# Optimization experiments

Hardware: AMD Instinct MI355X
Metric: run time of the kernel (lower is better)

The kernel has to match this reference:

```python
import jax, jax.numpy as jnp
import numpy as np

SEG_T = 0.7      # segmentation_map_threshold
GAUSS_T = 0.7    # gaussian_segmentation_threshold
EPS = 1e-07
PI_APPROX = 3.14  # literal used in the original code


def setup_inputs() -> dict:
    key = jax.random.key(0)
    k1, k2 = jax.random.split(key)
    B, H, W = 2, 80, 80
    variance_map = jax.random.normal(k1, (B, 3, H, W), dtype=jnp.float32)
    segmentation_map = jax.random.uniform(k2, (B, 1, H, W), dtype=jnp.float32)
    return {"variance_map": variance_map, "segmentation_map": segmentation_map}


def _splat_single(var, seg):
    # var: [3,H,W], seg: [H,W]
    H, W = seg.shape
    mask = (seg > SEG_T).reshape(-1)                      # [P], P = H*W (candidate points)
    vh = jnp.square(var[0].reshape(-1))                   # variance_height^2
    vw = jnp.square(var[1].reshape(-1))                   # variance_width^2
    th = PI_APPROX * jax.nn.sigmoid(var[2].reshape(-1))
    s, c = jnp.sin(th), jnp.cos(th)
    a = c * c / (2 * vh + EPS) + s * s / (2 * vw + EPS)
    b = -2 * s * c / (4 * vh + EPS) + 2 * s * c / (4 * vw + EPS)
    cc = s * s / (2 * vh + EPS) + c * c / (2 * vw + EPS)
    p = jnp.arange(H * W)
    x = (p // W).astype(jnp.float32)                      # row coordinate of each point
    y = (p % W).astype(jnp.float32)                       # col coordinate of each point
    ig, jg = jnp.meshgrid(jnp.arange(H, dtype=jnp.float32),
                          jnp.arange(W, dtype=jnp.float32), indexing="ij")
    di = ig[None, :, :] - x[:, None, None] + EPS          # [P,H,W]
    dj = jg[None, :, :] - y[:, None, None] + EPS          # [P,H,W]
    g = jnp.exp(-(a[:, None, None] * di * di
                  + b[:, None, None] * 2.0 * di * dj
                  + cc[:, None, None] * dj * dj) + EPS)   # [P,H,W]
    # zero out gaussians from points below the segmentation threshold;
    # since exp(.) > 0, this exactly matches max over only the nonzero points
    g = jnp.where(mask[:, None, None], g, 0.0)
    gmax = jnp.max(g, axis=0)                             # [H,W]
    return (gmax >= GAUSS_T).astype(gmax.dtype) * gmax


def reference(variance_map, segmentation_map):
    out = jax.vmap(_splat_single)(variance_map, segmentation_map[:, 0])  # [B,H,W]
    return out[:, None, :, :]                                            # [B,1,H,W]
```

## Files before the change

kernel.cpp:

```cpp
#include <hip/hip_runtime.h>
#include <math.h>

#define HGT 80
#define WID 80
#define HW 6400
#define SEG_T 0.7f
#define GAUSS_T 0.7f
#define EPSF 1e-7f
#define PI_APPROX 3.14f
#define EXP_CLAMP 85.0f
#define QKEEP 0.5f

#define NTHR 512
#define NWV  8
#define NIT  13

__global__ void __launch_bounds__(NTHR)
fused_kernel(const float* __restrict__ var, const float* __restrict__ seg,
             float* __restrict__ out) {
    __shared__ float qred[NWV][64];

    const int tid  = threadIdx.x;
    const int lane = tid & 63;
    const int wv   = tid >> 6;
    const int t    = blockIdx.x;
    const int b    = blockIdx.y;
    const int ti = t / 10, tj = t - ti * 10;
    const int pr = ti * 8 + (lane >> 3);
    const int pc = tj * 8 + (lane & 7);
    const float fi = (float)pr, fj = (float)pc;
    const float ii = fi * fi, ij = fi * fj, jj = fj * fj;
    const float tr0 = (float)(ti * 8), tr1 = (float)(ti * 8 + 7);
    const float tc0 = (float)(tj * 8), tc1 = (float)(tj * 8 + 7);

    const float* vb = var + (size_t)b * 3 * HW;
    const float* sg = seg + (size_t)b * HW;

    float qmin = 3.0e38f;

    for (int c = 0; c < NIT; ++c) {
        const int p = c * NTHR + tid;
        float C0, C1, C2, C3, C4, C5;
        bool keep = false;

        if (p < HW && sg[p] > SEG_T) {
            const float v0 = vb[p], v1 = vb[HW + p];
            const float vh = v0 * v0, vw = v1 * v1;
            const int rr = p / WID, ccol = p - rr * WID;
            const float x = (float)rr, y = (float)ccol;
            const float dx = fmaxf(0.0f, fmaxf(tr0 - x, x - tr1));
            const float dy = fmaxf(0.0f, fmaxf(tc0 - y, y - tc1));
            const float d2 = dx * dx + dy * dy;
            if (d2 <= QKEEP * (2.0f * fmaxf(vh, vw) + EPSF)) {
                const float v2 = vb[2 * HW + p];
                const float th = PI_APPROX * (1.0f / (1.0f + expf(-v2)));
                const float sn = sinf(th), cs = cosf(th);
                const float A  = cs * cs / (2.0f * vh + EPSF) + sn * sn / (2.0f * vw + EPSF);
                const float Bb = -2.0f * sn * cs / (4.0f * vh + EPSF)
                               +  2.0f * sn * cs / (4.0f * vw + EPSF);
                const float Cc = sn * sn / (2.0f * vh + EPSF) + cs * cs / (2.0f * vw + EPSF);
                const float B2 = 2.0f * Bb;
                const float u = EPSF - x;
                const float v = EPSF - y;
                C0 = A;
                C1 = B2;
                C2 = Cc;
                C3 = 2.0f * A * u + B2 * v;
                C4 = B2 * u + 2.0f * Cc * v;
                C5 = A * u * u + B2 * u * v + Cc * v * v;
                keep = true;
            }
        }

        unsigned long long msk = __ballot(keep);
        while (msk) {
            int s = (int)__builtin_ctzll(msk);
            msk &= msk - 1;
            float c0 = __shfl(C0, s), c1 = __shfl(C1, s);
            float c2 = __shfl(C2, s), c3 = __shfl(C3, s);
            float c4 = __shfl(C4, s), c5 = __shfl(C5, s);
            float Q = fmaf(c0, ii,
                      fmaf(c1, ij,
                      fmaf(c2, jj,
                      fmaf(c3, fi,
                      fmaf(c4, fj, c5)))));
            qmin = fminf(qmin, Q);
        }
    }

    qred[wv][lane] = qmin;
    __syncthreads();
    if (wv == 0) {
        float m2 = qred[0][lane];
        #pragma unroll
        for (int w = 1; w < NWV; ++w) m2 = fminf(m2, qred[w][lane]);
        float g = expf(fminf(EPSF - m2, EXP_CLAMP));
        out[(size_t)b * HW + pr * WID + pc] = (g >= GAUSS_T) ? g : 0.0f;
    }
}

extern "C" void kernel_launch(void* const* d_in, const int* in_sizes, int n_in,
                              void* d_out, int out_size, void* d_ws, size_t ws_size,
                              hipStream_t stream) {
    const float* var = (const float*)d_in[0];
    const float* seg = (const float*)d_in[1];
    float* out = (float*)d_out;
    int B = in_sizes[1] / HW;
    dim3 grid(100, B);
    fused_kernel<<<grid, NTHR, 0, stream>>>(var, seg, out);
}
```

Baseline: 63.84 us.

## Compact kept points into LDS list and compute coefficients densely per wave

Each wave first preloads seg and variance values for all its candidate points, then filters them and stream-compacts the survivors into a per-wave shared-memory index list using ballot and popcount. Gaussian coefficients are then computed once per batch of 64 kept points with full lane utilisation, replacing the sparse per-iteration divergent coefficient computation. The extra cost is shared memory (about 26KB for the list), more registers for the preloaded arrays, and a second gather of the variance values.

```diff
diff --git a/kernel.cpp b/kernel.cpp
--- a/kernel.cpp
+++ b/kernel.cpp
@@ -14,10 +14,12 @@
 #define NTHR 512
 #define NWV  8
 #define NIT  13
+#define QCAP (NIT*64)
 
 __global__ void __launch_bounds__(NTHR)
 fused_kernel(const float* __restrict__ var, const float* __restrict__ seg,
              float* __restrict__ out) {
+    __shared__ int   qlist[NWV][QCAP];
     __shared__ float qred[NWV][64];
 
     const int tid  = threadIdx.x;
@@ -36,54 +38,74 @@
     const float* vb = var + (size_t)b * 3 * HW;
     const float* sg = seg + (size_t)b * HW;
 
-    float qmin = 3.0e38f;
+    float sgv[NIT], av0[NIT], av1[NIT];
+    #pragma unroll
+    for (int c = 0; c < NIT; ++c) {
+        const int p  = c * NTHR + tid;
+        const int pk = (p < HW) ? p : (HW - 1);
+        sgv[c] = sg[pk];
+        av0[c] = vb[pk];
+        av1[c] = vb[HW + pk];
+    }
 
+    int qn = 0;
+    #pragma unroll
     for (int c = 0; c < NIT; ++c) {
         const int p = c * NTHR + tid;
-        float C0, C1, C2, C3, C4, C5;
         bool keep = false;
-
-        if (p < HW && sg[p] > SEG_T) {
-            const float v0 = vb[p], v1 = vb[HW + p];
-            const float vh = v0 * v0, vw = v1 * v1;
+        if (p < HW && sgv[c] > SEG_T) {
+            const float vh = av0[c] * av0[c], vw = av1[c] * av1[c];
             const int rr = p / WID, ccol = p - rr * WID;
             const float x = (float)rr, y = (float)ccol;
             const float dx = fmaxf(0.0f, fmaxf(tr0 - x, x - tr1));
             const float dy = fmaxf(0.0f, fmaxf(tc0 - y, y - tc1));
             const float d2 = dx * dx + dy * dy;
-            if (d2 <= QKEEP * (2.0f * fmaxf(vh, vw) + EPSF)) {
-                const float v2 = vb[2 * HW + p];
-                const float th = PI_APPROX * (1.0f / (1.0f + expf(-v2)));
-                const float sn = sinf(th), cs = cosf(th);
-                const float A  = cs * cs / (2.0f * vh + EPSF) + sn * sn / (2.0f * vw + EPSF);
-                const float Bb = -2.0f * sn * cs / (4.0f * vh + EPSF)
-                               +  2.0f * sn * cs / (4.0f * vw + EPSF);
-                const float Cc = sn * sn / (2.0f * vh + EPSF) + cs * cs / (2.0f * vw + EPSF);
-                const float B2 = 2.0f * Bb;
-                const float u = EPSF - x;
-                const float v = EPSF - y;
-                C0 = A;
-                C1 = B2;
-                C2 = Cc;
-                C3 = 2.0f * A * u + B2 * v;
-                C4 = B2 * u + 2.0f * Cc * v;
-                C5 = A * u * u + B2 * u * v + Cc * v * v;
-                keep = true;
+            keep = d2 <= QKEEP * (2.0f * fmaxf(vh, vw) + EPSF);
+        }
+        const unsigned long long msk = __ballot(keep);
+        if (msk) {
+            if (keep) {
+                const int idx = qn + (int)__popcll(msk & ((1ull << lane) - 1ull));
+                qlist[wv][idx] = p;
             }
+            qn += (int)__popcll(msk);
         }
+    }
 
-        unsigned long long msk = __ballot(keep);
-        while (msk) {
-            int s = (int)__builtin_ctzll(msk);
-            msk &= msk - 1;
-            float c0 = __shfl(C0, s), c1 = __shfl(C1, s);
-            float c2 = __shfl(C2, s), c3 = __shfl(C3, s);
-            float c4 = __shfl(C4, s), c5 = __shfl(C5, s);
-            float Q = fmaf(c0, ii,
-                      fmaf(c1, ij,
-                      fmaf(c2, jj,
-                      fmaf(c3, fi,
-                      fmaf(c4, fj, c5)))));
+    float qmin = 3.0e38f;
+    for (int base = 0; base < qn; base += 64) {
+        const int nb = min(64, qn - base);
+        float C0 = 0, C1 = 0, C2 = 0, C3 = 0, C4 = 0, C5 = 0;
+        if (lane < nb) {
+            const int p = qlist[wv][base + lane];
+            const float v0 = vb[p], v1 = vb[HW + p], v2 = vb[2 * HW + p];
+            const float vh = v0 * v0, vw = v1 * v1;
+            const float th = PI_APPROX * (1.0f / (1.0f + expf(-v2)));
+            const float sn = sinf(th), cs = cosf(th);
+            const float A  = cs * cs / (2.0f * vh + EPSF) + sn * sn / (2.0f * vw + EPSF);
+            const float Bb = -2.0f * sn * cs / (4.0f * vh + EPSF)
+                           +  2.0f * sn * cs / (4.0f * vw + EPSF);
+            const float Cc = sn * sn / (2.0f * vh + EPSF) + cs * cs / (2.0f * vw + EPSF);
+            const float B2 = 2.0f * Bb;
+            const int rr = p / WID, ccol = p - rr * WID;
+            const float u = EPSF - (float)rr;
+            const float v = EPSF - (float)ccol;
+            C0 = A;
+            C1 = B2;
+            C2 = Cc;
+            C3 = 2.0f * A * u + B2 * v;
+            C4 = B2 * u + 2.0f * Cc * v;
+            C5 = A * u * u + B2 * u * v + Cc * v * v;
+        }
+        for (int s = 0; s < nb; ++s) {
+            const float c0 = __shfl(C0, s), c1 = __shfl(C1, s);
+            const float c2 = __shfl(C2, s), c3 = __shfl(C3, s);
+            const float c4 = __shfl(C4, s), c5 = __shfl(C5, s);
+            const float Q = fmaf(c0, ii,
+                            fmaf(c1, ij,
+                            fmaf(c2, jj,
+                            fmaf(c3, fi,
+                            fmaf(c4, fj, c5)))));
             qmin = fminf(qmin, Q);
         }
     }
@@ -94,7 +116,7 @@
         float m2 = qred[0][lane];
         #pragma unroll
         for (int w = 1; w < NWV; ++w) m2 = fminf(m2, qred[w][lane]);
-        float g = expf(fminf(EPSF - m2, EXP_CLAMP));
+        const float g = expf(fminf(EPSF - m2, EXP_CLAMP));
         out[(size_t)b * HW + pr * WID + pc] = (g >= GAUSS_T) ? g : 0.0f;
     }
 }
```

New measurement: 58.76 us. 8.0% less time.
